# Performance work log

Measured on AMD Instinct MI355X. Metric: run time of the kernel, lower is better.

## Reference

```python
import jax, jax.numpy as jnp
import numpy as np

TEMPERATURE = 0.5  # init temperature; attn_drop=0.0 so dropout is identity


def setup_inputs() -> dict:
    key = jax.random.key(0)
    k1, k2, k3 = jax.random.split(key, 3)
    B, H, N, D = 4, 8, 2048, 64
    q = jax.random.normal(k1, (B, H, N, D), dtype=jnp.float32)
    k = jax.random.normal(k2, (B, H, N, D), dtype=jnp.float32)
    v = jax.random.normal(k3, (B, H, N, D), dtype=jnp.float32)
    scale = jnp.asarray(D ** -0.5, dtype=jnp.float32)
    return {"q": q, "k": k, "v": v, "scale": scale}


def reference(q, k, v, scale):
    # logits: [B,H,N,N]
    logits = jnp.einsum("bhqd,bhkd->bhqk", q, k) * scale
    # first softmax acts as a soft mask over keys
    soft_mask = jax.nn.softmax(logits / TEMPERATURE, axis=-1)
    # second softmax over masked logits (elementwise product, NOT matmul)
    attn = jax.nn.softmax(logits * soft_mask, axis=-1)
    # dropout with p=0.0 is identity
    out = jnp.einsum("bhqk,bhkd->bhqd", attn, v)
    return out
```

## Files before the change

kernel.cpp:

```cpp
#include <hip/hip_runtime.h>


typedef _Float16 f16;
typedef f16 f16x8 __attribute__((ext_vector_type(8)));
typedef float f32x4 __attribute__((ext_vector_type(4)));

#define MFMA(a, b, c) __builtin_amdgcn_mfma_f32_16x16x32_f16((a), (b), (c), 0, 0, 0)

#define N_CTX 2048
#define DH 64
#define KT 64
#define NKT (N_CTX / KT)
#define ROWS 128
#define QS 72

__device__ inline unsigned pk(float a, float b) {
    typedef __fp16 fp16x2_t __attribute__((ext_vector_type(2)));
    union { fp16x2_t v; unsigned u; } x;
    x.v = __builtin_amdgcn_cvt_pkrtz(a, b);
    return x.u;
}

__global__ __launch_bounds__(256, 2)
void stk_attn_mfma(const float* __restrict__ qg, const float* __restrict__ kg,
                   const float* __restrict__ vglob, const float* __restrict__ sg,
                   float* __restrict__ og) {
    __shared__ f16 Qs[ROWS * QS];
    __shared__ f16 Ks[KT * QS];
    __shared__ f16 Vt[DH * KT];
    __shared__ f16 Ps[4][32 * KT];

    const int tid  = threadIdx.x;
    const int wv   = tid >> 6;
    const int lane = tid & 63;
    const int l15  = lane & 15;
    const int q4   = lane >> 4;
    const int vp   = tid & 31;
    const int vgr  = tid >> 5;
    const int bh   = blockIdx.x >> 4;
    const int q0   = (blockIdx.x & 15) * ROWS;
    const float scale = sg[0];

    const float* qb = qg + (size_t)bh * N_CTX * DH;
    const float* kb = kg + (size_t)bh * N_CTX * DH;
    const float* vb = vglob + (size_t)bh * N_CTX * DH;
    float*       ob = og + (size_t)bh * N_CTX * DH;

    #pragma unroll
    for (int it = 0; it < 8; ++it) {
        int idx = it * 256 + tid;
        int row = idx >> 4, c4 = idx & 15;
        float4 v = *(const float4*)&qb[((size_t)(q0 + row)) * DH + c4 * 4];
        uint2 w = make_uint2(pk(v.x * scale, v.y * scale), pk(v.z * scale, v.w * scale));
        *(uint2*)&Qs[row * QS + c4 * 4] = w;
    }
    __syncthreads();

    f16x8 aq[2][2];
    #pragma unroll
    for (int rg = 0; rg < 2; ++rg)
        #pragma unroll
        for (int kc = 0; kc < 2; ++kc)
            aq[rg][kc] = *(const f16x8*)&Qs[(wv * 32 + rg * 16 + l15) * QS + kc * 32 + q4 * 8];

    float s1[8] = {0, 0, 0, 0, 0, 0, 0, 0};
    float4 kr[4];
    #pragma unroll
    for (int it = 0; it < 4; ++it) {
        int idx = it * 256 + tid;
        kr[it] = *(const float4*)&kb[((size_t)(idx >> 4)) * DH + (idx & 15) * 4];
    }
    for (int kt = 0; kt < NKT; ++kt) {
        __syncthreads();
        #pragma unroll
        for (int it = 0; it < 4; ++it) {
            int idx = it * 256 + tid;
            int row = idx >> 4, c4 = idx & 15;
            *(uint2*)&Ks[row * QS + c4 * 4] =
                make_uint2(pk(kr[it].x, kr[it].y), pk(kr[it].z, kr[it].w));
        }
        __syncthreads();
        if (kt + 1 < NKT) {
            #pragma unroll
            for (int it = 0; it < 4; ++it) {
                int idx = it * 256 + tid;
                kr[it] = *(const float4*)&kb[((size_t)(kt + 1) * KT + (idx >> 4)) * DH + (idx & 15) * 4];
            }
        }
        #pragma unroll
        for (int kgi = 0; kgi < 4; ++kgi) {
            f16x8 b0 = *(const f16x8*)&Ks[(kgi * 16 + l15) * QS + 0 * 32 + q4 * 8];
            f16x8 b1 = *(const f16x8*)&Ks[(kgi * 16 + l15) * QS + 1 * 32 + q4 * 8];
            #pragma unroll
            for (int rg = 0; rg < 2; ++rg) {
                f32x4 acc = {0.f, 0.f, 0.f, 0.f};
                acc = MFMA(aq[rg][0], b0, acc);
                acc = MFMA(aq[rg][1], b1, acc);
                #pragma unroll
                for (int r = 0; r < 4; ++r) {
                    float L = acc[r];
                    s1[rg * 4 + r] += __expf(L + L);
                }
            }
        }
    }
    float inv_s1[8];
    #pragma unroll
    for (int s = 0; s < 8; ++s) {
        float v = s1[s];
        v += __shfl_xor(v, 1, 64);
        v += __shfl_xor(v, 2, 64);
        v += __shfl_xor(v, 4, 64);
        v += __shfl_xor(v, 8, 64);
        inv_s1[s] = 1.0f / v;
    }

    float l2[8] = {0, 0, 0, 0, 0, 0, 0, 0};
    f32x4 O[2][4];
    #pragma unroll
    for (int rg = 0; rg < 2; ++rg)
        #pragma unroll
        for (int dt = 0; dt < 4; ++dt)
            O[rg][dt] = (f32x4){0.f, 0.f, 0.f, 0.f};

    float4 vr[4];
    #pragma unroll
    for (int it = 0; it < 4; ++it) {
        int idx = it * 256 + tid;
        kr[it] = *(const float4*)&kb[((size_t)(idx >> 4)) * DH + (idx & 15) * 4];
    }
    {
        const float* vs = vb + ((size_t)2 * vp) * DH + vgr * 8;
        vr[0] = *(const float4*)(vs);
        vr[1] = *(const float4*)(vs + 4);
        vr[2] = *(const float4*)(vs + DH);
        vr[3] = *(const float4*)(vs + DH + 4);
    }
    for (int kt = 0; kt < NKT; ++kt) {
        __syncthreads();
        #pragma unroll
        for (int it = 0; it < 4; ++it) {
            int idx = it * 256 + tid;
            int row = idx >> 4, c4 = idx & 15;
            *(uint2*)&Ks[row * QS + c4 * 4] =
                make_uint2(pk(kr[it].x, kr[it].y), pk(kr[it].z, kr[it].w));
        }
        #pragma unroll
        for (int j = 0; j < 4; ++j) {
            int d0 = vgr * 8 + j;
            int d1 = d0 + 4;
            float a0 = ((const float*)&vr[0])[j], c0 = ((const float*)&vr[2])[j];
            float a1 = ((const float*)&vr[1])[j], c1 = ((const float*)&vr[3])[j];
            *(unsigned*)&Vt[d0 * KT + ((2 * vp) ^ (8 * (d0 & 7)))] = pk(a0, c0);
            *(unsigned*)&Vt[d1 * KT + ((2 * vp) ^ (8 * (d1 & 7)))] = pk(a1, c1);
        }
        __syncthreads();
        if (kt + 1 < NKT) {
            #pragma unroll
            for (int it = 0; it < 4; ++it) {
                int idx = it * 256 + tid;
                kr[it] = *(const float4*)&kb[((size_t)(kt + 1) * KT + (idx >> 4)) * DH + (idx & 15) * 4];
            }
            const float* vs = vb + ((size_t)(kt + 1) * KT + 2 * vp) * DH + vgr * 8;
            vr[0] = *(const float4*)(vs);
            vr[1] = *(const float4*)(vs + 4);
            vr[2] = *(const float4*)(vs + DH);
            vr[3] = *(const float4*)(vs + DH + 4);
        }

        #pragma unroll
        for (int kgi = 0; kgi < 4; ++kgi) {
            f16x8 b0 = *(const f16x8*)&Ks[(kgi * 16 + l15) * QS + 0 * 32 + q4 * 8];
            f16x8 b1 = *(const f16x8*)&Ks[(kgi * 16 + l15) * QS + 1 * 32 + q4 * 8];
            #pragma unroll
            for (int rg = 0; rg < 2; ++rg) {
                f32x4 acc = {0.f, 0.f, 0.f, 0.f};
                acc = MFMA(aq[rg][0], b0, acc);
                acc = MFMA(aq[rg][1], b1, acc);
                #pragma unroll
                for (int r = 0; r < 4; ++r) {
                    float L  = acc[r];
                    float e1 = __expf(L + L);
                    float w  = e1 * inv_s1[rg * 4 + r];
                    float e2 = __expf(L * w);
                    l2[rg * 4 + r] += e2;
                    int lrow = rg * 16 + q4 * 4 + r;
                    int col  = kgi * 16 + l15;
                    Ps[wv][lrow * KT + (col ^ ((lrow & 7) * 8))] = (f16)e2;
                }
            }
        }
        #pragma unroll
        for (int kc = 0; kc < 2; ++kc) {
            int kbase = kc * 32 + q4 * 8;
            f16x8 ap0 = *(const f16x8*)&Ps[wv][(0 + l15) * KT + (kbase ^ ((l15 & 7) * 8))];
            f16x8 ap1 = *(const f16x8*)&Ps[wv][(16 + l15) * KT + (kbase ^ ((l15 & 7) * 8))];
            #pragma unroll
            for (int dt = 0; dt < 4; ++dt) {
                f16x8 bv = *(const f16x8*)&Vt[(dt * 16 + l15) * KT + (kbase ^ ((l15 & 7) * 8))];
                O[0][dt] = MFMA(ap0, bv, O[0][dt]);
                O[1][dt] = MFMA(ap1, bv, O[1][dt]);
            }
        }
    }

    float inv_l2[8];
    #pragma unroll
    for (int s = 0; s < 8; ++s) {
        float v = l2[s];
        v += __shfl_xor(v, 1, 64);
        v += __shfl_xor(v, 2, 64);
        v += __shfl_xor(v, 4, 64);
        v += __shfl_xor(v, 8, 64);
        inv_l2[s] = 1.0f / v;
    }
    #pragma unroll
    for (int rg = 0; rg < 2; ++rg)
        #pragma unroll
        for (int dt = 0; dt < 4; ++dt)
            #pragma unroll
            for (int r = 0; r < 4; ++r) {
                int row = q0 + wv * 32 + rg * 16 + q4 * 4 + r;
                ob[(size_t)row * DH + dt * 16 + l15] = O[rg][dt][r] * inv_l2[rg * 4 + r];
            }
}

extern "C" void kernel_launch(void* const* d_in, const int* in_sizes, int n_in,
                              void* d_out, int out_size, void* d_ws, size_t ws_size,
                              hipStream_t stream) {
    const float* q = (const float*)d_in[0];
    const float* k = (const float*)d_in[1];
    const float* v = (const float*)d_in[2];
    const float* s = (const float*)d_in[3];
    float* out = (float*)d_out;
    dim3 grid(32 * 16);
    stk_attn_mfma<<<grid, 256, 0, stream>>>(q, k, v, s, out);
}
```

Before: 197.3 us.

## Use 512-thread blocks with 16 rows per wave and exp2-based softmax

Blocks now have 8 waves of 16 query rows each instead of 4 waves of 32 rows, so each wave keeps half the accumulators and Q fragments, and the launch bound asks for 4 blocks per CU. The exponentials use the hardware exp2 with the log2(e) factors folded into the constants and the reciprocal. The block-to-(head, query tile) mapping is also reordered so neighbouring blocks fall on different heads. The aim is more latency hiding and less transcendental overhead. The cost is that each K/V tile staged in shared memory is reused by fewer rows per wave, and B-operand LDS reads per MFMA double.

```diff
diff --git a/kernel.cpp b/kernel.cpp
--- a/kernel.cpp
+++ b/kernel.cpp
@@ -6,6 +6,7 @@
 typedef float f32x4 __attribute__((ext_vector_type(4)));
 
 #define MFMA(a, b, c) __builtin_amdgcn_mfma_f32_16x16x32_f16((a), (b), (c), 0, 0, 0)
+#define EXP2(x) __builtin_amdgcn_exp2f(x)
 
 #define N_CTX 2048
 #define DH 64
@@ -14,6 +15,9 @@
 #define ROWS 128
 #define QS 72
 
+#define C2  2.885390081777927f
+#define L2E 1.442695040888963f
+
 __device__ inline unsigned pk(float a, float b) {
     typedef __fp16 fp16x2_t __attribute__((ext_vector_type(2)));
     union { fp16x2_t v; unsigned u; } x;
@@ -21,14 +25,14 @@
     return x.u;
 }
 
-__global__ __launch_bounds__(256, 2)
+__global__ __launch_bounds__(512, 4)
 void stk_attn_mfma(const float* __restrict__ qg, const float* __restrict__ kg,
                    const float* __restrict__ vglob, const float* __restrict__ sg,
                    float* __restrict__ og) {
     __shared__ f16 Qs[ROWS * QS];
     __shared__ f16 Ks[KT * QS];
     __shared__ f16 Vt[DH * KT];
-    __shared__ f16 Ps[4][32 * KT];
+    __shared__ f16 Ps[8][16 * KT];
 
     const int tid  = threadIdx.x;
     const int wv   = tid >> 6;
@@ -37,8 +41,8 @@
     const int q4   = lane >> 4;
     const int vp   = tid & 31;
     const int vgr  = tid >> 5;
-    const int bh   = blockIdx.x >> 4;
-    const int q0   = (blockIdx.x & 15) * ROWS;
+    const int bh   = blockIdx.x & 31;
+    const int q0   = (blockIdx.x >> 5) * ROWS;
     const float scale = sg[0];
 
     const float* qb = qg + (size_t)bh * N_CTX * DH;
@@ -47,34 +51,32 @@
     float*       ob = og + (size_t)bh * N_CTX * DH;
 
     #pragma unroll
-    for (int it = 0; it < 8; ++it) {
-        int idx = it * 256 + tid;
+    for (int it = 0; it < 4; ++it) {
+        int idx = it * 512 + tid;
         int row = idx >> 4, c4 = idx & 15;
         float4 v = *(const float4*)&qb[((size_t)(q0 + row)) * DH + c4 * 4];
-        uint2 w = make_uint2(pk(v.x * scale, v.y * scale), pk(v.z * scale, v.w * scale));
-        *(uint2*)&Qs[row * QS + c4 * 4] = w;
+        *(uint2*)&Qs[row * QS + c4 * 4] =
+            make_uint2(pk(v.x * scale, v.y * scale), pk(v.z * scale, v.w * scale));
     }
     __syncthreads();
 
-    f16x8 aq[2][2];
-    #pragma unroll
-    for (int rg = 0; rg < 2; ++rg)
-        #pragma unroll
-        for (int kc = 0; kc < 2; ++kc)
-            aq[rg][kc] = *(const f16x8*)&Qs[(wv * 32 + rg * 16 + l15) * QS + kc * 32 + q4 * 8];
-
-    float s1[8] = {0, 0, 0, 0, 0, 0, 0, 0};
-    float4 kr[4];
-    #pragma unroll
-    for (int it = 0; it < 4; ++it) {
-        int idx = it * 256 + tid;
+    f16x8 aq[2];
+    #pragma unroll
+    for (int kc = 0; kc < 2; ++kc)
+        aq[kc] = *(const f16x8*)&Qs[(wv * 16 + l15) * QS + kc * 32 + q4 * 8];
+
+    float s1[4] = {0, 0, 0, 0};
+    float4 kr[2];
+    #pragma unroll
+    for (int it = 0; it < 2; ++it) {
+        int idx = it * 512 + tid;
         kr[it] = *(const float4*)&kb[((size_t)(idx >> 4)) * DH + (idx & 15) * 4];
     }
     for (int kt = 0; kt < NKT; ++kt) {
         __syncthreads();
         #pragma unroll
-        for (int it = 0; it < 4; ++it) {
-            int idx = it * 256 + tid;
+        for (int it = 0; it < 2; ++it) {
+            int idx = it * 512 + tid;
             int row = idx >> 4, c4 = idx & 15;
             *(uint2*)&Ks[row * QS + c4 * 4] =
                 make_uint2(pk(kr[it].x, kr[it].y), pk(kr[it].z, kr[it].w));
@@ -82,8 +84,8 @@
         __syncthreads();
         if (kt + 1 < NKT) {
             #pragma unroll
-            for (int it = 0; it < 4; ++it) {
-                int idx = it * 256 + tid;
+            for (int it = 0; it < 2; ++it) {
+                int idx = it * 512 + tid;
                 kr[it] = *(const float4*)&kb[((size_t)(kt + 1) * KT + (idx >> 4)) * DH + (idx & 15) * 4];
             }
         }
@@ -91,138 +93,116 @@
         for (int kgi = 0; kgi < 4; ++kgi) {
             f16x8 b0 = *(const f16x8*)&Ks[(kgi * 16 + l15) * QS + 0 * 32 + q4 * 8];
             f16x8 b1 = *(const f16x8*)&Ks[(kgi * 16 + l15) * QS + 1 * 32 + q4 * 8];
-            #pragma unroll
-            for (int rg = 0; rg < 2; ++rg) {
-                f32x4 acc = {0.f, 0.f, 0.f, 0.f};
-                acc = MFMA(aq[rg][0], b0, acc);
-                acc = MFMA(aq[rg][1], b1, acc);
-                #pragma unroll
-                for (int r = 0; r < 4; ++r) {
-                    float L = acc[r];
-                    s1[rg * 4 + r] += __expf(L + L);
-                }
-            }
-        }
-    }
-    float inv_s1[8];
-    #pragma unroll
-    for (int s = 0; s < 8; ++s) {
+            f32x4 acc = {0.f, 0.f, 0.f, 0.f};
+            acc = MFMA(aq[0], b0, acc);
+            acc = MFMA(aq[1], b1, acc);
+            #pragma unroll
+            for (int r = 0; r < 4; ++r)
+                s1[r] += EXP2(acc[r] * C2);
+        }
+    }
+    float inv1[4];
+    #pragma unroll
+    for (int s = 0; s < 4; ++s) {
         float v = s1[s];
         v += __shfl_xor(v, 1, 64);
         v += __shfl_xor(v, 2, 64);
         v += __shfl_xor(v, 4, 64);
         v += __shfl_xor(v, 8, 64);
-        inv_s1[s] = 1.0f / v;
-    }
-
-    float l2[8] = {0, 0, 0, 0, 0, 0, 0, 0};
-    f32x4 O[2][4];
-    #pragma unroll
-    for (int rg = 0; rg < 2; ++rg)
-        #pragma unroll
-        for (int dt = 0; dt < 4; ++dt)
-            O[rg][dt] = (f32x4){0.f, 0.f, 0.f, 0.f};
-
-    float4 vr[4];
-    #pragma unroll
-    for (int it = 0; it < 4; ++it) {
-        int idx = it * 256 + tid;
+        inv1[s] = L2E / v;
+    }
+
+    float l2[4] = {0, 0, 0, 0};
+    f32x4 O[4];
+    #pragma unroll
+    for (int dt = 0; dt < 4; ++dt) O[dt] = (f32x4){0.f, 0.f, 0.f, 0.f};
+
+    float4 vr[2];
+    #pragma unroll
+    for (int it = 0; it < 2; ++it) {
+        int idx = it * 512 + tid;
         kr[it] = *(const float4*)&kb[((size_t)(idx >> 4)) * DH + (idx & 15) * 4];
     }
     {
-        const float* vs = vb + ((size_t)2 * vp) * DH + vgr * 8;
+        const float* vs = vb + ((size_t)2 * vp) * DH + vgr * 4;
         vr[0] = *(const float4*)(vs);
-        vr[1] = *(const float4*)(vs + 4);
-        vr[2] = *(const float4*)(vs + DH);
-        vr[3] = *(const float4*)(vs + DH + 4);
+        vr[1] = *(const float4*)(vs + DH);
     }
     for (int kt = 0; kt < NKT; ++kt) {
         __syncthreads();
         #pragma unroll
-        for (int it = 0; it < 4; ++it) {
-            int idx = it * 256 + tid;
+        for (int it = 0; it < 2; ++it) {
+            int idx = it * 512 + tid;
             int row = idx >> 4, c4 = idx & 15;
             *(uint2*)&Ks[row * QS + c4 * 4] =
                 make_uint2(pk(kr[it].x, kr[it].y), pk(kr[it].z, kr[it].w));
         }
         #pragma unroll
         for (int j = 0; j < 4; ++j) {
-            int d0 = vgr * 8 + j;
-            int d1 = d0 + 4;
-            float a0 = ((const float*)&vr[0])[j], c0 = ((const float*)&vr[2])[j];
-            float a1 = ((const float*)&vr[1])[j], c1 = ((const float*)&vr[3])[j];
-            *(unsigned*)&Vt[d0 * KT + ((2 * vp) ^ (8 * (d0 & 7)))] = pk(a0, c0);
-            *(unsigned*)&Vt[d1 * KT + ((2 * vp) ^ (8 * (d1 & 7)))] = pk(a1, c1);
+            int d = vgr * 4 + j;
+            float a0 = ((const float*)&vr[0])[j];
+            float a1 = ((const float*)&vr[1])[j];
+            *(unsigned*)&Vt[d * KT + ((2 * vp) ^ (8 * (d & 7)))] = pk(a0, a1);
         }
         __syncthreads();
         if (kt + 1 < NKT) {
             #pragma unroll
-            for (int it = 0; it < 4; ++it) {
-                int idx = it * 256 + tid;
+            for (int it = 0; it < 2; ++it) {
+                int idx = it * 512 + tid;
                 kr[it] = *(const float4*)&kb[((size_t)(kt + 1) * KT + (idx >> 4)) * DH + (idx & 15) * 4];
             }
-            const float* vs = vb + ((size_t)(kt + 1) * KT + 2 * vp) * DH + vgr * 8;
+            const float* vs = vb + ((size_t)(kt + 1) * KT + 2 * vp) * DH + vgr * 4;
             vr[0] = *(const float4*)(vs);
-            vr[1] = *(const float4*)(vs + 4);
-            vr[2] = *(const float4*)(vs + DH);
-            vr[3] = *(const float4*)(vs + DH + 4);
+            vr[1] = *(const float4*)(vs + DH);
         }
 
         #pragma unroll
         for (int kgi = 0; kgi < 4; ++kgi) {
             f16x8 b0 = *(const f16x8*)&Ks[(kgi * 16 + l15) * QS + 0 * 32 + q4 * 8];
             f16x8 b1 = *(const f16x8*)&Ks[(kgi * 16 + l15) * QS + 1 * 32 + q4 * 8];
-            #pragma unroll
-            for (int rg = 0; rg < 2; ++rg) {
-                f32x4 acc = {0.f, 0.f, 0.f, 0.f};
-                acc = MFMA(aq[rg][0], b0, acc);
-                acc = MFMA(aq[rg][1], b1, acc);
-                #pragma unroll
-                for (int r = 0; r < 4; ++r) {
-                    float L  = acc[r];
-                    float e1 = __expf(L + L);
-                    float w  = e1 * inv_s1[rg * 4 + r];
-                    float e2 = __expf(L * w);
-                    l2[rg * 4 + r] += e2;
-                    int lrow = rg * 16 + q4 * 4 + r;
-                    int col  = kgi * 16 + l15;
-                    Ps[wv][lrow * KT + (col ^ ((lrow & 7) * 8))] = (f16)e2;
-                }
+            f32x4 acc = {0.f, 0.f, 0.f, 0.f};
+            acc = MFMA(aq[0], b0, acc);
+            acc = MFMA(aq[1], b1, acc);
+            #pragma unroll
+            for (int r = 0; r < 4; ++r) {
+                float L  = acc[r];
+                float e1 = EXP2(L * C2);
+                float e2 = EXP2((L * e1) * inv1[r]);
+                l2[r] += e2;
+                int lrow = q4 * 4 + r;
+                int col  = kgi * 16 + l15;
+                Ps[wv][lrow * KT + (col ^ ((lrow & 7) * 8))] = (f16)e2;
             }
         }
         #pragma unroll
         for (int kc = 0; kc < 2; ++kc) {
             int kbase = kc * 32 + q4 * 8;
-            f16x8 ap0 = *(const f16x8*)&Ps[wv][(0 + l15) * KT + (kbase ^ ((l15 & 7) * 8))];
-            f16x8 ap1 = *(const f16x8*)&Ps[wv][(16 + l15) * KT + (kbase ^ ((l15 & 7) * 8))];
+            f16x8 ap = *(const f16x8*)&Ps[wv][l15 * KT + (kbase ^ ((l15 & 7) * 8))];
             #pragma unroll
             for (int dt = 0; dt < 4; ++dt) {
                 f16x8 bv = *(const f16x8*)&Vt[(dt * 16 + l15) * KT + (kbase ^ ((l15 & 7) * 8))];
-                O[0][dt] = MFMA(ap0, bv, O[0][dt]);
-                O[1][dt] = MFMA(ap1, bv, O[1][dt]);
-            }
-        }
-    }
-
-    float inv_l2[8];
-    #pragma unroll
-    for (int s = 0; s < 8; ++s) {
+                O[dt] = MFMA(ap, bv, O[dt]);
+            }
+        }
+    }
+
+    float invl2[4];
+    #pragma unroll
+    for (int s = 0; s < 4; ++s) {
         float v = l2[s];
         v += __shfl_xor(v, 1, 64);
         v += __shfl_xor(v, 2, 64);
         v += __shfl_xor(v, 4, 64);
         v += __shfl_xor(v, 8, 64);
-        inv_l2[s] = 1.0f / v;
-    }
-    #pragma unroll
-    for (int rg = 0; rg < 2; ++rg)
-        #pragma unroll
-        for (int dt = 0; dt < 4; ++dt)
-            #pragma unroll
-            for (int r = 0; r < 4; ++r) {
-                int row = q0 + wv * 32 + rg * 16 + q4 * 4 + r;
-                ob[(size_t)row * DH + dt * 16 + l15] = O[rg][dt][r] * inv_l2[rg * 4 + r];
-            }
+        invl2[s] = 1.0f / v;
+    }
+    #pragma unroll
+    for (int dt = 0; dt < 4; ++dt)
+        #pragma unroll
+        for (int r = 0; r < 4; ++r) {
+            int row = q0 + wv * 16 + q4 * 4 + r;
+            ob[(size_t)row * DH + dt * 16 + l15] = O[dt][r] * invl2[r];
+        }
 }
 
 extern "C" void kernel_launch(void* const* d_in, const int* in_sizes, int n_in,
@@ -234,5 +214,5 @@
     const float* s = (const float*)d_in[3];
     float* out = (float*)d_out;
     dim3 grid(32 * 16);
-    stk_attn_mfma<<<grid, 256, 0, stream>>>(q, k, v, s, out);
+    stk_attn_mfma<<<grid, 512, 0, stream>>>(q, k, v, s, out);
 }
```

Result: faster. 181.7 us (-7.9%).
